# Performance work log

Measured on AMD Instinct MI355X. Metric: run time of the kernel, lower is better.

## Reference

```python
import jax, jax.numpy as jnp
import numpy as np

N_NODES = 50000
N_EDGES = 800000
N_GRAPHS = 256
VOCAB = 40
EMB = 128
HID = 256
NCLS = 10


def setup_inputs() -> dict:
    key = jax.random.key(0)
    ks = jax.random.split(key, 12)
    x = jax.random.randint(ks[0], (N_NODES,), 0, VOCAB)
    edge_index = jax.random.randint(ks[1], (2, N_EDGES), 0, N_NODES)
    batch = jnp.sort(jax.random.randint(ks[2], (N_NODES,), 0, N_GRAPHS))

    def init(k, shape, fan_in):
        return jax.random.normal(k, shape, jnp.float32) * (1.0 / np.sqrt(fan_in))

    return {
        "x": x,
        "edge_index": edge_index,
        "batch": batch,
        "emb": init(ks[3], (VOCAB, EMB), EMB),
        "W1l": init(ks[4], (EMB, HID), EMB),
        "W1r": init(ks[5], (EMB, HID), EMB),
        "b1": jnp.zeros((HID,), jnp.float32),
        "W2l": init(ks[6], (HID, HID), HID),
        "W2r": init(ks[7], (HID, HID), HID),
        "b2": jnp.zeros((HID,), jnp.float32),
        "Wo": init(ks[8], (HID, NCLS), HID),
        "bo": jnp.zeros((NCLS,), jnp.float32),
    }


def _segment_mean(v, ids, n):
    # v: [M, D], ids: [M] -> [n, D] mean per segment (empty segments -> 0)
    s = jax.ops.segment_sum(v, ids, num_segments=n)
    c = jax.ops.segment_sum(jnp.ones((ids.shape[0], 1), v.dtype), ids, num_segments=n)
    return s / jnp.maximum(c, 1.0)


def _sage_conv(h, src, dst, Wl, Wr, b):
    # PyG SAGEConv: lin_l(mean of neighbor msgs) + lin_r(self) + bias
    mean_nb = _segment_mean(h[src], dst, h.shape[0])  # [N, D_in]
    return mean_nb @ Wl + h @ Wr + b


def reference(x, edge_index, batch, emb, W1l, W1r, b1, W2l, W2r, b2, Wo, bo):
    src, dst = edge_index[0], edge_index[1]
    h = emb[x]                                          # [N, EMB]
    h = jax.nn.relu(_sage_conv(h, src, dst, W1l, W1r, b1))  # [N, HID]
    h = jax.nn.relu(_sage_conv(h, src, dst, W2l, W2r, b2))  # [N, HID]
    g = _segment_mean(h, batch, N_GRAPHS)               # [G, HID]
    return g @ Wo + bo                                  # [G, NCLS]
```

## Files before the change

kernel.cpp:

```cpp
#include <hip/hip_runtime.h>
#include <hip/hip_bf16.h>

#define N_NODES 50000
#define N_EDGES 800000
#define N_GRAPHS 256
#define EMB 128
#define HID 256
#define NCLS 10
#define VOCAB 40
#define NPAD 50048
#define DMAX 64

typedef __attribute__((ext_vector_type(4))) float f32x4;
typedef __attribute__((ext_vector_type(8))) _Float16 f16x8;
typedef __attribute__((ext_vector_type(4))) _Float16 f16x4;
typedef unsigned int u32;
#define AS1 __attribute__((address_space(1)))
#define AS3 __attribute__((address_space(3)))

__device__ __forceinline__ int imax(int a, int b) { return a > b ? a : b; }
__device__ __forceinline__ int imin(int a, int b) { return a < b ? a : b; }
__device__ __forceinline__ float bf2f(ushort h) { return __uint_as_float(((unsigned)h) << 16); }


__global__ void zero_k(int* __restrict__ p, int n, const unsigned short* __restrict__ w,
                       int* __restrict__ flag) {
    int i = blockIdx.x * blockDim.x + threadIdx.x;
    if (i < n) p[i] = 0;
    if (i == 0) {
        int ok = 1;
        for (int j = 0; j < 64; ++j) {
            float f = __uint_as_float(((unsigned)w[j]) << 16);
            if (!(fabsf(f) < 16.0f)) { ok = 0; break; }
        }
        *flag = ok;
    }
}

struct ConvArgs { const void* src[7]; int dstoff[7]; int cum[8]; };

__global__ void convert_k(ConvArgs a, float* __restrict__ dst, const int* __restrict__ flag) {
    int bf = *flag;
    int i = blockIdx.x * blockDim.x + threadIdx.x;
    if (i >= a.cum[7]) return;
    int s = 0;
    while (i >= a.cum[s + 1]) ++s;
    int j = i - a.cum[s];
    float v;
    if (bf) v = bf2f(((const unsigned short*)a.src[s])[j]);
    else    v = ((const float*)a.src[s])[j];
    dst[a.dstoff[s] + j] = v;
}

__global__ void pack_w2_k(const void* __restrict__ W2l, const void* __restrict__ W2r,
                          const int* __restrict__ flag, _Float16* __restrict__ W2t) {
    int bf = *flag;
    int i = blockIdx.x * 256 + threadIdx.x;
    int n = i >> 9, k = i & 511;
    const void* p = (k < 256) ? W2l : W2r;
    int idx = ((k & 255) * 256) + n;
    float v;
    if (bf) v = bf2f(((const unsigned short*)p)[idx]);
    else    v = ((const float*)p)[idx];
    W2t[(size_t)n * 512 + k] = (_Float16)v;
}

__global__ void ew_k(const float* __restrict__ Wf, _Float16* __restrict__ EWt,
                     float* __restrict__ EW2) {
    int v = blockIdx.x, n = threadIdx.x;
    if (v >= VOCAB) { EWt[n * 64 + v] = (_Float16)0.f; return; }
    const float* er = Wf + v * EMB;
    float a = 0.f, b = 0.f;
    for (int k = 0; k < EMB; ++k) {
        float ev = er[k];
        a = fmaf(ev, Wf[5120 + k * 256 + n], a);
        b = fmaf(ev, Wf[37888 + k * 256 + n], b);
    }
    EWt[n * 64 + v] = (_Float16)a;
    EW2[v * 256 + n] = b;
}

__global__ void gbound_k(const int* __restrict__ batch, int* __restrict__ gstart) {
    int i = blockIdx.x * blockDim.x + threadIdx.x;
    if (i < N_NODES) {
        int b = batch[i];
        int bp = (i == 0) ? -1 : batch[i - 1];
        for (int g = bp + 1; g <= b; ++g) gstart[g] = i;
        if (i == N_NODES - 1)
            for (int g = b + 1; g <= N_GRAPHS; ++g) gstart[g] = N_NODES;
    }
}

__global__ void scatter_k(const int* __restrict__ src, const int* __restrict__ dst,
                          int* __restrict__ nxt, ushort* __restrict__ col) {
    int e = blockIdx.x * blockDim.x + threadIdx.x;
    if (e < N_EDGES) {
        int d = dst[e];
        int p = atomicAdd(&nxt[d], 1);
        if (p < DMAX) col[d * DMAX + p] = (ushort)src[e];
    }
}

__global__ void ct2_k(const int* __restrict__ deg, const ushort* __restrict__ colv,
                      const int* __restrict__ x, char* __restrict__ Ct) {
    __shared__ ushort cnt[VOCAB * 256];
    int tid = threadIdx.x;
    int nl = tid >> 2, sub = tid & 3;
    int n = blockIdx.x * 64 + nl;
#pragma unroll
    for (int v = 0; v < VOCAB; ++v) cnt[v * 256 + tid] = 0;
    if (n < N_NODES) {
        int s0 = n * DMAX;
        int s1 = s0 + imin(deg[n], DMAX);
        for (int e = s0 + sub; e < s1; e += 4) {
            int v = x[colv[e]];
            cnt[v * 256 + tid]++;
        }
    }
    __syncthreads();
    if (tid < 64) {
        int nn = blockIdx.x * 64 + tid;
        char* tile = Ct + (size_t)(nn >> 6) * 8192 + (nn & 63) * 128;
        int xorb = nn & 7;
#pragma unroll
        for (int b = 0; b < 8; ++b) {
            int kbase = (b ^ xorb) * 8;
            f16x8 o;
#pragma unroll
            for (int j = 0; j < 8; ++j) {
                int k = kbase + j;
                int c = 0;
                if (k < VOCAB)
                    c = cnt[k * 256 + tid * 4 + 0] + cnt[k * 256 + tid * 4 + 1] +
                        cnt[k * 256 + tid * 4 + 2] + cnt[k * 256 + tid * 4 + 3];
                o[j] = (_Float16)(float)c;
            }
            *(f16x8*)(tile + b * 16) = o;
        }
    }
}

__global__ __launch_bounds__(256, 2) void gemm1_k(
    const char* __restrict__ Ct, const _Float16* __restrict__ EWt,
    const float* __restrict__ EW2, const int* __restrict__ xv,
    const int* __restrict__ deg, const float* __restrict__ bias,
    char* __restrict__ E) {
    __shared__ __attribute__((aligned(16))) char As[8192];
    const int tid = threadIdx.x, wave = tid >> 6, lane = tid & 63;
    const int row0 = blockIdx.x * 64, col0 = wave * 64;
    const char* sp = Ct + (size_t)blockIdx.x * 8192 + tid * 16;
    __builtin_amdgcn_global_load_lds((const AS1 u32*)sp, (AS3 u32*)(As + tid * 16), 16, 0, 0);
    __builtin_amdgcn_global_load_lds((const AS1 u32*)(sp + 4096),
                                     (AS3 u32*)(As + tid * 16 + 4096), 16, 0, 0);
    f16x8 B[8];
#pragma unroll
    for (int n = 0; n < 4; ++n) {
        const _Float16* wp = EWt + (size_t)(col0 + n * 16 + (lane & 15)) * 64 + ((lane >> 4) * 8);
        B[n] = *(const f16x8*)wp;
        B[4 + n] = *(const f16x8*)(wp + 32);
    }
    int offA[2][4];
#pragma unroll
    for (int h = 0; h < 2; ++h)
#pragma unroll
        for (int m = 0; m < 4; ++m) {
            int r = (lane & 15) + m * 16;
            int b = h * 64 + (lane >> 4) * 16;
            offA[h][m] = r * 128 + (b ^ ((r & 7) << 4));
        }
    f32x4 acc[4][4];
#pragma unroll
    for (int m = 0; m < 4; ++m)
#pragma unroll
        for (int n = 0; n < 4; ++n) acc[m][n] = (f32x4){0.f, 0.f, 0.f, 0.f};
    asm volatile("s_waitcnt vmcnt(0)" ::: "memory");
    __syncthreads();
#pragma unroll
    for (int h = 0; h < 2; ++h) {
        f16x8 a[4];
#pragma unroll
        for (int m = 0; m < 4; ++m) a[m] = *(const f16x8*)(As + offA[h][m]);
#pragma unroll
        for (int m = 0; m < 4; ++m)
#pragma unroll
            for (int n = 0; n < 4; ++n)
                acc[m][n] = __builtin_amdgcn_mfma_f32_16x16x32_f16(a[m], B[h * 4 + n],
                                                                   acc[m][n], 0, 0, 0);
    }
    int rbase = row0 + ((lane >> 4) * 4);
    int cbase = col0 + (lane & 15);
    float bv[4];
#pragma unroll
    for (int n = 0; n < 4; ++n) bv[n] = bias[cbase + n * 16];
#pragma unroll
    for (int m = 0; m < 4; ++m)
#pragma unroll
        for (int r = 0; r < 4; ++r) {
            int row = rbase + m * 16 + r;
            if (row < N_NODES) {
                float invd = 1.f / (float)imax(deg[row], 1);
                const float* e2 = EW2 + (size_t)xv[row] * 256;
#pragma unroll
                for (int n = 0; n < 4; ++n) {
                    int colc = cbase + n * 16;
                    float v = acc[m][n][r] * invd + e2[colc] + bv[n];
                    v = v > 0.f ? v : 0.f;
                    char* ep = E + ((size_t)(row >> 6) * 8 + 4 + (colc >> 6)) * 8192 +
                               (row & 63) * 128 + (((colc & 63) * 2) ^ ((row & 7) << 4));
                    *(_Float16*)ep = (_Float16)v;
                }
            }
        }
}

__global__ void agg2_k(const int* __restrict__ deg, const ushort* __restrict__ colv,
                       char* __restrict__ A2c) {
    int w = (blockIdx.x * blockDim.x + threadIdx.x) >> 6;
    int lane = threadIdx.x & 63;
    if (w >= N_NODES) return;
    int dg = deg[w];
    int s0 = w * DMAX, s1 = s0 + imin(dg, DMAX);
    int ktof = 4 + (lane >> 4);
    int bof = (lane & 15) * 8;
    float ac0 = 0.f, ac1 = 0.f, ac2 = 0.f, ac3 = 0.f;
#define ADDR2(s) (A2c + ((size_t)((s) >> 6) * 8 + ktof) * 8192 + ((s) & 63) * 128 + \
                  (bof ^ (((s) & 7) << 4)))
    int e = s0;
    for (; e + 4 <= s1; e += 4) {
        int sA = colv[e], sB = colv[e + 1], sC = colv[e + 2], sD = colv[e + 3];
        f16x4 h0 = *(const f16x4*)ADDR2(sA);
        f16x4 h1 = *(const f16x4*)ADDR2(sB);
        f16x4 h2 = *(const f16x4*)ADDR2(sC);
        f16x4 h3 = *(const f16x4*)ADDR2(sD);
        ac0 += (float)h0[0] + (float)h1[0] + (float)h2[0] + (float)h3[0];
        ac1 += (float)h0[1] + (float)h1[1] + (float)h2[1] + (float)h3[1];
        ac2 += (float)h0[2] + (float)h1[2] + (float)h2[2] + (float)h3[2];
        ac3 += (float)h0[3] + (float)h1[3] + (float)h2[3] + (float)h3[3];
    }
    for (; e < s1; ++e) {
        f16x4 hv = *(const f16x4*)ADDR2(colv[e]);
        ac0 += (float)hv[0];
        ac1 += (float)hv[1];
        ac2 += (float)hv[2];
        ac3 += (float)hv[3];
    }
#undef ADDR2
    float inv = 1.f / (float)imax(dg, 1);
    f16x4 o;
    o[0] = (_Float16)(ac0 * inv);
    o[1] = (_Float16)(ac1 * inv);
    o[2] = (_Float16)(ac2 * inv);
    o[3] = (_Float16)(ac3 * inv);
    char* mp = A2c + ((size_t)(w >> 6) * 8 + (ktof - 4)) * 8192 + (w & 63) * 128 +
               (bof ^ ((w & 7) << 4));
    *(f16x4*)mp = o;
}

template <int K>
__global__ __launch_bounds__(256, 2) void gemm2_k(
    const char* __restrict__ Aswz, const _Float16* __restrict__ Wt,
    const float* __restrict__ bias, const int* __restrict__ batch,
    float* __restrict__ g_acc) {
    constexpr int NT = K / 64;
    __shared__ __attribute__((aligned(16))) char As[4 * 8192];
    const int tid = threadIdx.x, wave = tid >> 6, lane = tid & 63;
    const int row0 = blockIdx.x * 64, col0 = wave * 64;
    const char* Ab = Aswz + (size_t)blockIdx.x * NT * 8192 + tid * 16;
    const _Float16* Wp = Wt + (size_t)(col0 + (lane & 15)) * K + ((lane >> 4) * 8);

    int offA[2][4];
#pragma unroll
    for (int h = 0; h < 2; ++h)
#pragma unroll
        for (int m = 0; m < 4; ++m) {
            int r = (lane & 15) + m * 16;
            int b = h * 64 + (lane >> 4) * 16;
            offA[h][m] = r * 128 + (b ^ ((r & 7) << 4));
        }

    f32x4 acc[4][4];
#pragma unroll
    for (int m = 0; m < 4; ++m)
#pragma unroll
        for (int n = 0; n < 4; ++n) acc[m][n] = (f32x4){0.f, 0.f, 0.f, 0.f};

    f16x8 B0[8], B1[8];

#define STAGE(t)                                                                     \
    {                                                                                \
        const char* _s = Ab + (size_t)(t) * 8192;                                    \
        char* _d = As + ((t) & 3) * 8192 + tid * 16;                                 \
        __builtin_amdgcn_global_load_lds((const AS1 u32*)_s, (AS3 u32*)_d, 16, 0, 0);\
        __builtin_amdgcn_global_load_lds((const AS1 u32*)(_s + 4096),                \
                                         (AS3 u32*)(_d + 4096), 16, 0, 0);           \
    }
#define LOADB(t, Bf)                                                                 \
    {                                                                                \
        _Pragma("unroll") for (int n = 0; n < 4; ++n) {                              \
            Bf[n]     = *(const f16x8*)(Wp + (size_t)n * 16 * K + (t) * 64);         \
            Bf[4 + n] = *(const f16x8*)(Wp + (size_t)n * 16 * K + (t) * 64 + 32);    \
        }                                                                            \
    }
#define COMP(p, Bf)                                                                  \
    {                                                                                \
        const char* _b = As + (p) * 8192;                                            \
        _Pragma("unroll") for (int h = 0; h < 2; ++h) {                              \
            f16x8 _a[4];                                                             \
            _Pragma("unroll") for (int m = 0; m < 4; ++m)                            \
                _a[m] = *(const f16x8*)(_b + offA[h][m]);                            \
            _Pragma("unroll") for (int m = 0; m < 4; ++m)                            \
                _Pragma("unroll") for (int n = 0; n < 4; ++n)                        \
                    acc[m][n] = __builtin_amdgcn_mfma_f32_16x16x32_f16(              \
                        _a[m], Bf[h * 4 + n], acc[m][n], 0, 0, 0);                   \
        }                                                                            \
    }
#define WAITBAR()                                                                    \
    {                                                                                \
        asm volatile("s_waitcnt vmcnt(12)" ::: "memory");                            \
        __builtin_amdgcn_s_barrier();                                                \
        asm volatile("" ::: "memory");                                               \
    }

    STAGE(0);
    LOADB(0, B0);
    STAGE(1);
    STAGE(2);

#pragma unroll 1
    for (int t = 0; t < NT; t += 2) {
        WAITBAR();
        if (t + 3 < NT) STAGE(t + 3);
        LOADB(t + 1, B1);
        COMP(t & 3, B0);
        WAITBAR();
        if (t + 4 < NT) STAGE(t + 4);
        if (t + 2 < NT) LOADB(t + 2, B0);
        COMP((t + 1) & 3, B1);
    }

    __syncthreads();
    float bv[4];
#pragma unroll
    for (int n = 0; n < 4; ++n) bv[n] = bias[col0 + n * 16 + (lane & 15)];
    int rloc = (lane >> 4) * 4;
    int cbase = col0 + (lane & 15);
#pragma unroll
    for (int m = 0; m < 4; ++m)
#pragma unroll
        for (int n = 0; n < 4; ++n)
#pragma unroll
            for (int r = 0; r < 4; ++r) {
                float v = acc[m][n][r] + bv[n];
                v = v > 0.f ? v : 0.f;
                *(_Float16*)(As + (rloc + m * 16 + r) * 512 + (cbase + n * 16) * 2) =
                    (_Float16)v;
            }
    __syncthreads();
    int rmax = imin(64, N_NODES - row0);
    int cur = batch[row0];
    float run = 0.f;
    for (int r = 0; r < rmax; ++r) {
        int b = batch[row0 + r];
        if (b != cur) {
            atomicAdd(&g_acc[cur * HID + tid], run);
            run = 0.f;
            cur = b;
        }
        run += (float)*(const _Float16*)(As + r * 512 + tid * 2);
    }
    atomicAdd(&g_acc[cur * HID + tid], run);
#undef STAGE
#undef LOADB
#undef COMP
#undef WAITBAR
}

__global__ void final_k(const float* __restrict__ g_acc, const int* __restrict__ gstart,
                        const float* __restrict__ Wo, const float* __restrict__ bo,
                        void* __restrict__ out, const int* __restrict__ flag) {
    __shared__ float gm[HID];
    __shared__ float red[HID];
    int g = blockIdx.x, t = threadIdx.x;
    int cnt = gstart[g + 1] - gstart[g];
    float inv = 1.0f / (float)imax(cnt, 1);
    gm[t] = g_acc[g * HID + t] * inv;
    __syncthreads();
    int bf = *flag;
    for (int c = 0; c < NCLS; ++c) {
        red[t] = gm[t] * Wo[t * NCLS + c];
        __syncthreads();
        for (int s = HID / 2; s > 0; s >>= 1) {
            if (t < s) red[t] += red[t + s];
            __syncthreads();
        }
        if (t == 0) {
            float o = red[0] + bo[c];
            if (bf) ((__hip_bfloat16*)out)[g * NCLS + c] = __float2bfloat16(o);
            else    ((float*)out)[g * NCLS + c] = o;
        }
        __syncthreads();
    }
}

extern "C" void kernel_launch(void* const* d_in, const int* in_sizes, int n_in,
                              void* d_out, int out_size, void* d_ws, size_t ws_size,
                              hipStream_t stream) {
    const int* x     = (const int*)d_in[0];
    const int* ei    = (const int*)d_in[1];
    const int* batch = (const int*)d_in[2];
    const int* srcp = ei;
    const int* dstp = ei + N_EDGES;

    char* w = (char*)d_ws;
    auto alloc = [&](size_t bytes) -> char* {
        char* p = w;
        w += (bytes + 255) & ~(size_t)255;
        return p;
    };
    int* flag = (int*)alloc(256);
    const int ZWORDS = N_NODES + N_GRAPHS * HID;
    int* zbase = (int*)alloc((size_t)ZWORDS * 4);
    int* nxt = zbase;
    float* g_acc = (float*)(zbase + N_NODES);
    int* gstart  = (int*)alloc((size_t)(N_GRAPHS + 1) * 4);
    ushort* col  = (ushort*)alloc((size_t)N_NODES * DMAX * 2);
    float* Wf    = (float*)alloc((size_t)204810 * 4);
    _Float16* W2t = (_Float16*)alloc((size_t)256 * 512 * 2);
    _Float16* EWt = (_Float16*)alloc((size_t)256 * 64 * 2);
    float* EW2    = (float*)alloc((size_t)VOCAB * 256 * 4);
    char* Ct      = alloc((size_t)(NPAD / 64) * 8192);
    char* A2c     = alloc((size_t)(NPAD / 64) * 8 * 8192);
    alloc(4096);

    float* b1 = Wf + 70656;
    float* b2 = Wf + 201984;
    float* Wo = Wf + 202240;
    float* bo = Wf + 204800;

    zero_k<<<(ZWORDS + 255) / 256, 256, 0, stream>>>(zbase, ZWORDS,
                                                     (const unsigned short*)d_in[3], flag);

    ConvArgs ca;
    const void* csrc[7] = {d_in[3], d_in[4], d_in[5], d_in[6], d_in[9], d_in[10], d_in[11]};
    const int clen[7]  = {5120, 32768, 32768, 256, 256, 2560, 10};
    const int cdst[7]  = {0, 5120, 37888, 70656, 201984, 202240, 204800};
    int acc = 0;
    for (int i = 0; i < 7; ++i) {
        ca.src[i] = csrc[i];
        ca.dstoff[i] = cdst[i];
        ca.cum[i] = acc;
        acc += clen[i];
    }
    ca.cum[7] = acc;
    convert_k<<<(acc + 255) / 256, 256, 0, stream>>>(ca, Wf, flag);

    pack_w2_k<<<512, 256, 0, stream>>>(d_in[7], d_in[8], flag, W2t);
    ew_k<<<64, 256, 0, stream>>>(Wf, EWt, EW2);
    gbound_k<<<(N_NODES + 255) / 256, 256, 0, stream>>>(batch, gstart);

    scatter_k<<<(N_EDGES + 255) / 256, 256, 0, stream>>>(srcp, dstp, nxt, col);

    const int GB = NPAD / 64;
    ct2_k<<<GB, 256, 0, stream>>>(nxt, col, x, Ct);

    gemm1_k<<<GB, 256, 0, stream>>>(Ct, EWt, EW2, x, nxt, b1, A2c);
    agg2_k<<<(N_NODES * 64 + 255) / 256, 256, 0, stream>>>(nxt, col, A2c);
    gemm2_k<512><<<GB, 256, 0, stream>>>(A2c, W2t, b2, batch, g_acc);

    final_k<<<N_GRAPHS, HID, 0, stream>>>(g_acc, gstart, Wo, bo, d_out, flag);

    (void)in_sizes; (void)n_in; (void)out_size; (void)ws_size;
}
```

Measured before the change: 201.9 us.

## Build adjacency via LDS histogram counting sort and merge prep kernels

Replaces the global-atomic edge scatter with a three-pass counting sort. It builds per-block LDS histograms of packed 16-bit counts, takes an exclusive scan across blocks, then places edges deterministically. It also merges the zero, convert, pack, embedding-weight product and graph-bound kernels into one prep kernel, and has each consumer detect bf16 inline instead of reading a flag. The aim is to remove contended global atomics and several launches. In exchange it adds extra passes over the edges, a 6.4MB count buffer and per-thread repeated bf16 detection.

```diff
diff --git a/kernel.cpp b/kernel.cpp
--- a/kernel.cpp
+++ b/kernel.cpp
@@ -2,14 +2,17 @@
 #include <hip/hip_bf16.h>
 
 #define N_NODES 50000
-#define N_EDGES 800000
 #define N_GRAPHS 256
 #define EMB 128
 #define HID 256
 #define NCLS 10
 #define VOCAB 40
 #define NPAD 50048
+#define NROW 50048
 #define DMAX 64
+#define NEDGE 800000
+#define P1B 64
+#define EPB 12500
 
 typedef __attribute__((ext_vector_type(4))) float f32x4;
 typedef __attribute__((ext_vector_type(8))) _Float16 f16x8;
@@ -22,82 +25,135 @@
 __device__ __forceinline__ int imin(int a, int b) { return a < b ? a : b; }
 __device__ __forceinline__ float bf2f(ushort h) { return __uint_as_float(((unsigned)h) << 16); }
 
-
-__global__ void zero_k(int* __restrict__ p, int n, const unsigned short* __restrict__ w,
-                       int* __restrict__ flag) {
-    int i = blockIdx.x * blockDim.x + threadIdx.x;
-    if (i < n) p[i] = 0;
-    if (i == 0) {
-        int ok = 1;
-        for (int j = 0; j < 64; ++j) {
-            float f = __uint_as_float(((unsigned)w[j]) << 16);
-            if (!(fabsf(f) < 16.0f)) { ok = 0; break; }
-        }
-        *flag = ok;
-    }
-}
-
-struct ConvArgs { const void* src[7]; int dstoff[7]; int cum[8]; };
-
-__global__ void convert_k(ConvArgs a, float* __restrict__ dst, const int* __restrict__ flag) {
-    int bf = *flag;
-    int i = blockIdx.x * blockDim.x + threadIdx.x;
-    if (i >= a.cum[7]) return;
-    int s = 0;
-    while (i >= a.cum[s + 1]) ++s;
-    int j = i - a.cum[s];
-    float v;
-    if (bf) v = bf2f(((const unsigned short*)a.src[s])[j]);
-    else    v = ((const float*)a.src[s])[j];
-    dst[a.dstoff[s] + j] = v;
-}
-
-__global__ void pack_w2_k(const void* __restrict__ W2l, const void* __restrict__ W2r,
-                          const int* __restrict__ flag, _Float16* __restrict__ W2t) {
-    int bf = *flag;
-    int i = blockIdx.x * 256 + threadIdx.x;
-    int n = i >> 9, k = i & 511;
-    const void* p = (k < 256) ? W2l : W2r;
-    int idx = ((k & 255) * 256) + n;
-    float v;
-    if (bf) v = bf2f(((const unsigned short*)p)[idx]);
-    else    v = ((const float*)p)[idx];
-    W2t[(size_t)n * 512 + k] = (_Float16)v;
-}
-
-__global__ void ew_k(const float* __restrict__ Wf, _Float16* __restrict__ EWt,
-                     float* __restrict__ EW2) {
-    int v = blockIdx.x, n = threadIdx.x;
-    if (v >= VOCAB) { EWt[n * 64 + v] = (_Float16)0.f; return; }
-    const float* er = Wf + v * EMB;
-    float a = 0.f, b = 0.f;
-    for (int k = 0; k < EMB; ++k) {
-        float ev = er[k];
-        a = fmaf(ev, Wf[5120 + k * 256 + n], a);
-        b = fmaf(ev, Wf[37888 + k * 256 + n], b);
-    }
-    EWt[n * 64 + v] = (_Float16)a;
-    EW2[v * 256 + n] = b;
-}
-
-__global__ void gbound_k(const int* __restrict__ batch, int* __restrict__ gstart) {
-    int i = blockIdx.x * blockDim.x + threadIdx.x;
-    if (i < N_NODES) {
-        int b = batch[i];
-        int bp = (i == 0) ? -1 : batch[i - 1];
-        for (int g = bp + 1; g <= b; ++g) gstart[g] = i;
-        if (i == N_NODES - 1)
-            for (int g = b + 1; g <= N_GRAPHS; ++g) gstart[g] = N_NODES;
-    }
-}
-
-__global__ void scatter_k(const int* __restrict__ src, const int* __restrict__ dst,
-                          int* __restrict__ nxt, ushort* __restrict__ col) {
-    int e = blockIdx.x * blockDim.x + threadIdx.x;
-    if (e < N_EDGES) {
+__device__ __forceinline__ int detect_bf16(const unsigned short* w) {
+    int ok = 1;
+#pragma unroll
+    for (int i = 0; i < 64; ++i) {
+        float f = __uint_as_float(((unsigned)w[i]) << 16);
+        ok &= (fabsf(f) < 16.0f) ? 1 : 0;
+    }
+    return ok;
+}
+__device__ __forceinline__ float ldw(const void* p, int idx, int bf) {
+    if (bf) return bf2f(((const unsigned short*)p)[idx]);
+    return ((const float*)p)[idx];
+}
+
+
+struct PrepArgs {
+    const void* bsrc[4];
+    const unsigned short* emb16;
+    const void* W1l; const void* W1r;
+    const void* W2l; const void* W2r;
+    const int* batch;
+    float* Wb;
+    _Float16* W2t;
+    _Float16* EWt;
+    float* EW2;
+    int* gstart;
+    float* g_acc;
+};
+
+__global__ void prep_k(PrepArgs a) {
+    int b = blockIdx.x, t = threadIdx.x;
+    if (b < 13) {
+        int i = b * 256 + t;
+        if (i < 3082) {
+            int bf = detect_bf16(a.emb16);
+            const int cum[5] = {0, 256, 512, 3072, 3082};
+            int s = 0;
+            while (i >= cum[s + 1]) ++s;
+            a.Wb[i] = ldw(a.bsrc[s], i - cum[s], bf);
+        }
+    } else if (b < 525) {
+        int bf = detect_bf16(a.emb16);
+        int j = (b - 13) * 256 + t;
+        int n = j >> 9, k = j & 511;
+        const void* p = (k < 256) ? a.W2l : a.W2r;
+        a.W2t[(size_t)n * 512 + k] = (_Float16)ldw(p, (k & 255) * 256 + n, bf);
+    } else if (b < 589) {
+        int v = b - 525, n = t;
+        if (v >= VOCAB) { a.EWt[n * 64 + v] = (_Float16)0.f; return; }
+        int bf = detect_bf16(a.emb16);
+        float s1 = 0.f, s2 = 0.f;
+        for (int k = 0; k < EMB; ++k) {
+            float ev = ldw(a.emb16, v * EMB + k, bf);
+            s1 = fmaf(ev, ldw(a.W1l, k * 256 + n, bf), s1);
+            s2 = fmaf(ev, ldw(a.W1r, k * 256 + n, bf), s2);
+        }
+        a.EWt[n * 64 + v] = (_Float16)s1;
+        a.EW2[v * 256 + n] = s2;
+    } else if (b < 785) {
+        int i = (b - 589) * 256 + t;
+        if (i < N_NODES) {
+            int bb = a.batch[i];
+            int bp = (i == 0) ? -1 : a.batch[i - 1];
+            for (int g = bp + 1; g <= bb; ++g) a.gstart[g] = i;
+            if (i == N_NODES - 1)
+                for (int g = bb + 1; g <= N_GRAPHS; ++g) a.gstart[g] = N_NODES;
+        }
+    } else {
+        int i = (b - 785) * 256 + t;
+        if (i < N_GRAPHS * HID) a.g_acc[i] = 0.f;
+    }
+}
+
+__global__ __launch_bounds__(1024) void p1_k(const int* __restrict__ dst,
+                                             ushort* __restrict__ erank,
+                                             ushort* __restrict__ cnts) {
+    __shared__ u32 h[NROW / 2];
+    int tid = threadIdx.x, blk = blockIdx.x;
+    for (int w = tid; w < NROW / 2; w += 1024) h[w] = 0;
+    __syncthreads();
+    int base = blk * EPB;
+    for (int i = tid; i < EPB; i += 1024) {
+        int e = base + i;
         int d = dst[e];
-        int p = atomicAdd(&nxt[d], 1);
-        if (p < DMAX) col[d * DMAX + p] = (ushort)src[e];
+        u32 sh = (u32)(d & 1) * 16u;
+        u32 old = atomicAdd(&h[d >> 1], 1u << sh);
+        erank[e] = (ushort)((old >> sh) & 0xffffu);
+    }
+    __syncthreads();
+    u32* crow = (u32*)(cnts + (size_t)blk * NROW);
+    for (int w = tid; w < NROW / 2; w += 1024) crow[w] = h[w];
+}
+
+__global__ __launch_bounds__(512) void p2_k(ushort* __restrict__ cnts,
+                                            int* __restrict__ deg) {
+    __shared__ ushort c[P1B][512];
+    int t = threadIdx.x, nb = blockIdx.x * 512;
+    int n = nb + t;
+    bool ok = (n < NROW);
+    for (int b = 0; b < P1B; ++b)
+        c[b][t] = ok ? cnts[(size_t)b * NROW + n] : (ushort)0;
+    int run = 0;
+    for (int b = 0; b < P1B; ++b) {
+        int v = c[b][t];
+        c[b][t] = (ushort)run;
+        run += v;
+    }
+    if (ok) {
+        deg[n] = run;
+        for (int b = 0; b < P1B; ++b) cnts[(size_t)b * NROW + n] = c[b][t];
+    }
+}
+
+__global__ __launch_bounds__(1024) void p3_k(const int* __restrict__ src,
+                                             const int* __restrict__ dst,
+                                             const ushort* __restrict__ erank,
+                                             const ushort* __restrict__ offs,
+                                             ushort* __restrict__ col) {
+    __shared__ ushort off_l[NROW];
+    int tid = threadIdx.x, blk = blockIdx.x;
+    const ushort* orow = offs + (size_t)blk * NROW;
+    for (int w = tid; w < NROW; w += 1024) off_l[w] = orow[w];
+    __syncthreads();
+    int base = blk * EPB;
+    for (int i = tid; i < EPB; i += 1024) {
+        int e = base + i;
+        int d = dst[e];
+        int p = (int)off_l[d] + (int)erank[e];
+        if (p < DMAX) col[(size_t)d * DMAX + p] = (ushort)src[e];
     }
 }
 
@@ -377,7 +433,7 @@
 
 __global__ void final_k(const float* __restrict__ g_acc, const int* __restrict__ gstart,
                         const float* __restrict__ Wo, const float* __restrict__ bo,
-                        void* __restrict__ out, const int* __restrict__ flag) {
+                        void* __restrict__ out, const unsigned short* __restrict__ emb16) {
     __shared__ float gm[HID];
     __shared__ float red[HID];
     int g = blockIdx.x, t = threadIdx.x;
@@ -385,7 +441,7 @@
     float inv = 1.0f / (float)imax(cnt, 1);
     gm[t] = g_acc[g * HID + t] * inv;
     __syncthreads();
-    int bf = *flag;
+    int bf = detect_bf16(emb16);
     for (int c = 0; c < NCLS; ++c) {
         red[t] = gm[t] * Wo[t * NCLS + c];
         __syncthreads();
@@ -409,7 +465,7 @@
     const int* ei    = (const int*)d_in[1];
     const int* batch = (const int*)d_in[2];
     const int* srcp = ei;
-    const int* dstp = ei + N_EDGES;
+    const int* dstp = ei + NEDGE;
 
     char* w = (char*)d_ws;
     auto alloc = [&](size_t bytes) -> char* {
@@ -417,14 +473,13 @@
         w += (bytes + 255) & ~(size_t)255;
         return p;
     };
-    int* flag = (int*)alloc(256);
-    const int ZWORDS = N_NODES + N_GRAPHS * HID;
-    int* zbase = (int*)alloc((size_t)ZWORDS * 4);
-    int* nxt = zbase;
-    float* g_acc = (float*)(zbase + N_NODES);
+    float* g_acc = (float*)alloc((size_t)N_GRAPHS * HID * 4);
+    int* deg     = (int*)alloc((size_t)NROW * 4);
     int* gstart  = (int*)alloc((size_t)(N_GRAPHS + 1) * 4);
-    ushort* col  = (ushort*)alloc((size_t)N_NODES * DMAX * 2);
-    float* Wf    = (float*)alloc((size_t)204810 * 4);
+    ushort* erank = (ushort*)alloc((size_t)NEDGE * 2);
+    ushort* cnts  = (ushort*)alloc((size_t)P1B * NROW * 2);
+    ushort* col   = (ushort*)alloc((size_t)N_NODES * DMAX * 2);
+    float* Wb     = (float*)alloc((size_t)3328 * 4);
     _Float16* W2t = (_Float16*)alloc((size_t)256 * 512 * 2);
     _Float16* EWt = (_Float16*)alloc((size_t)256 * 64 * 2);
     float* EW2    = (float*)alloc((size_t)VOCAB * 256 * 4);
@@ -432,42 +487,28 @@
     char* A2c     = alloc((size_t)(NPAD / 64) * 8 * 8192);
     alloc(4096);
 
-    float* b1 = Wf + 70656;
-    float* b2 = Wf + 201984;
-    float* Wo = Wf + 202240;
-    float* bo = Wf + 204800;
-
-    zero_k<<<(ZWORDS + 255) / 256, 256, 0, stream>>>(zbase, ZWORDS,
-                                                     (const unsigned short*)d_in[3], flag);
-
-    ConvArgs ca;
-    const void* csrc[7] = {d_in[3], d_in[4], d_in[5], d_in[6], d_in[9], d_in[10], d_in[11]};
-    const int clen[7]  = {5120, 32768, 32768, 256, 256, 2560, 10};
-    const int cdst[7]  = {0, 5120, 37888, 70656, 201984, 202240, 204800};
-    int acc = 0;
-    for (int i = 0; i < 7; ++i) {
-        ca.src[i] = csrc[i];
-        ca.dstoff[i] = cdst[i];
-        ca.cum[i] = acc;
-        acc += clen[i];
-    }
-    ca.cum[7] = acc;
-    convert_k<<<(acc + 255) / 256, 256, 0, stream>>>(ca, Wf, flag);
-
-    pack_w2_k<<<512, 256, 0, stream>>>(d_in[7], d_in[8], flag, W2t);
-    ew_k<<<64, 256, 0, stream>>>(Wf, EWt, EW2);
-    gbound_k<<<(N_NODES + 255) / 256, 256, 0, stream>>>(batch, gstart);
-
-    scatter_k<<<(N_EDGES + 255) / 256, 256, 0, stream>>>(srcp, dstp, nxt, col);
+    PrepArgs pa;
+    pa.bsrc[0] = d_in[6];  pa.bsrc[1] = d_in[9];
+    pa.bsrc[2] = d_in[10]; pa.bsrc[3] = d_in[11];
+    pa.emb16 = (const unsigned short*)d_in[3];
+    pa.W1l = d_in[4]; pa.W1r = d_in[5];
+    pa.W2l = d_in[7]; pa.W2r = d_in[8];
+    pa.batch = batch;
+    pa.Wb = Wb; pa.W2t = W2t; pa.EWt = EWt; pa.EW2 = EW2;
+    pa.gstart = gstart; pa.g_acc = g_acc;
+    prep_k<<<1041, 256, 0, stream>>>(pa);
+
+    p1_k<<<P1B, 1024, 0, stream>>>(dstp, erank, cnts);
+    p2_k<<<(NROW + 511) / 512, 512, 0, stream>>>(cnts, deg);
+    p3_k<<<P1B, 1024, 0, stream>>>(srcp, dstp, erank, cnts, col);
 
     const int GB = NPAD / 64;
-    ct2_k<<<GB, 256, 0, stream>>>(nxt, col, x, Ct);
-
-    gemm1_k<<<GB, 256, 0, stream>>>(Ct, EWt, EW2, x, nxt, b1, A2c);
-    agg2_k<<<(N_NODES * 64 + 255) / 256, 256, 0, stream>>>(nxt, col, A2c);
-    gemm2_k<512><<<GB, 256, 0, stream>>>(A2c, W2t, b2, batch, g_acc);
-
-    final_k<<<N_GRAPHS, HID, 0, stream>>>(g_acc, gstart, Wo, bo, d_out, flag);
+    ct2_k<<<GB, 256, 0, stream>>>(deg, col, x, Ct);
+    gemm1_k<<<GB, 256, 0, stream>>>(Ct, EWt, EW2, x, deg, Wb, A2c);
+    agg2_k<<<(N_NODES * 64 + 255) / 256, 256, 0, stream>>>(deg, col, A2c);
+    gemm2_k<512><<<GB, 256, 0, stream>>>(A2c, W2t, Wb + 256, batch, g_acc);
+    final_k<<<N_GRAPHS, HID, 0, stream>>>(g_acc, gstart, Wb + 512, Wb + 3072, d_out,
+                                          (const unsigned short*)d_in[3]);
 
     (void)in_sizes; (void)n_in; (void)out_size; (void)ws_size;
 }
```

Result: slower. 221.1 us (+9.5%).
